# Optimization experiments

Hardware: AMD Instinct MI355X
Metric: run time of the kernel (lower is better)

## Reference

```python
import jax, jax.numpy as jnp
import numpy as np

Nc, Np = 100_000, 200_000
E = 1_000_000
D_IN, C, H = 64, 128, 8
D = C // H  # per-head dim = 16
NEG_SLOPE = 0.2
BN_EPS = 1e-5


def setup_inputs() -> dict:
    key = jax.random.key(0)
    ks = jax.random.split(key, 24)
    rn = lambda i, shape, s=0.05: jax.random.normal(ks[i], shape, jnp.float32) * s
    inp = {
        'x_customer': jax.random.normal(ks[0], (Nc, D_IN), jnp.float32),
        'x_product': jax.random.normal(ks[1], (Np, D_IN), jnp.float32),
        'edge_src_cp': jax.random.randint(ks[2], (E,), 0, Nc),
        'edge_dst_cp': jax.random.randint(ks[3], (E,), 0, Np),
        'edge_src_pp': jax.random.randint(ks[4], (E,), 0, Np),
        'edge_dst_pp': jax.random.randint(ks[5], (E,), 0, Np),
        # HANConv per-node-type projections
        'W_c': rn(6, (D_IN, C)), 'b_c': jnp.zeros((C,), jnp.float32),
        'W_p': rn(7, (D_IN, C)), 'b_p': jnp.zeros((C,), jnp.float32),
        # per-edge-type attention vectors [H, D]
        'a_src_cp': rn(8, (H, D), 0.2), 'a_dst_cp': rn(9, (H, D), 0.2),
        'a_src_pp': rn(10, (H, D), 0.2), 'a_dst_pp': rn(11, (H, D), 0.2),
        # semantic attention (k_lin + q)
        'Wk': rn(12, (C, C)), 'bk': jnp.zeros((C,), jnp.float32),
        'q_sem': rn(13, (C,), 0.2),
        # MLP head + BN params
        'W1': rn(14, (C, 128)), 'b1': jnp.zeros((128,), jnp.float32),
        'g1': jnp.ones((128,), jnp.float32), 'be1': jnp.zeros((128,), jnp.float32),
        'W2': rn(15, (128, 64)), 'b2': jnp.zeros((64,), jnp.float32),
        'g2': jnp.ones((64,), jnp.float32), 'be2': jnp.zeros((64,), jnp.float32),
        'W3': rn(16, (64, 1)), 'b3': jnp.zeros((1,), jnp.float32),
    }
    return inp


def _edge_type_attention(h_src, h_dst, a_src, a_dst, e_src, e_dst, n_dst):
    # h_src: [N_src, H, D]; per-node attention logits [N, H]
    al_src = jnp.sum(h_src * a_src, axis=-1)
    al_dst = jnp.sum(h_dst * a_dst, axis=-1)
    al = al_src[e_src] + al_dst[e_dst]                      # [E, H]
    al = jnp.where(al >= 0, al, NEG_SLOPE * al)             # leaky_relu
    m = jax.ops.segment_max(al, e_dst, num_segments=n_dst)  # [n_dst, H]
    m = jnp.where(jnp.isfinite(m), m, 0.0)                  # empty segments
    ex = jnp.exp(al - m[e_dst])
    s = jax.ops.segment_sum(ex, e_dst, num_segments=n_dst)
    alpha = ex / (s[e_dst] + 1e-16)                         # [E, H]
    msg = h_src[e_src] * alpha[..., None]                   # [E, H, D]
    out = jax.ops.segment_sum(msg, e_dst, num_segments=n_dst)
    return jax.nn.relu(out.reshape(n_dst, H * D))


def _bn(x, g, b):
    mu = jnp.mean(x, axis=0)
    var = jnp.var(x, axis=0)
    return g * (x - mu) * jax.lax.rsqrt(var + BN_EPS) + b


def reference(x_customer, x_product, W_c, b_c, W_p, b_p,
              a_src_cp, a_dst_cp, a_src_pp, a_dst_pp,
              Wk, bk, q_sem,
              W1, b1, g1, be1, W2, b2, g2, be2, W3, b3,
              edge_src_cp, edge_dst_cp, edge_src_pp, edge_dst_pp):
    # node-type projections -> [N, H, D]
    h_c = (x_customer @ W_c + b_c).reshape(Nc, H, D)
    h_p = (x_product @ W_p + b_p).reshape(Np, H, D)
    # per-edge-type multi-head attention into 'product_order'
    out_cp = _edge_type_attention(h_c, h_p, a_src_cp, a_dst_cp, edge_src_cp, edge_dst_cp, Np)
    out_pp = _edge_type_attention(h_p, h_p, a_src_pp, a_dst_pp, edge_src_pp, edge_dst_pp, Np)
    # semantic attention over the 2 metapaths
    outs = jnp.stack([out_cp, out_pp])                      # [2, Np, C]
    k = jnp.mean(jnp.tanh(outs @ Wk + bk), axis=1)          # [2, C]
    attn = jax.nn.softmax(jnp.sum(k * q_sem, axis=-1))      # [2]
    out = jnp.sum(attn[:, None, None] * outs, axis=0)       # [Np, C]
    # MLP head (dropout disabled; BN uses batch statistics)
    h = jax.nn.relu(_bn(out @ W1 + b1, g1, be1))
    h = jax.nn.relu(_bn(h @ W2 + b2, g2, be2))
    return jax.nn.sigmoid(h @ W3 + b3)
```

## Files before the change

### kernel.cpp

```cpp
#include <hip/hip_runtime.h>
#include <hip/hip_bf16.h>

#define NC 100000
#define NP 200000
#define NE 1000000
#define NN2 (2 * NP)
#define NBUK 391
#define ECHUNK 8192
#define NBLK_E 245
#define NTILE 3125
#define SEMB 782

typedef unsigned short u16;
typedef unsigned int u32;
typedef unsigned long long u64;
typedef __attribute__((ext_vector_type(8))) short short8v;
typedef __attribute__((ext_vector_type(4))) float f32x4;

__device__ __forceinline__ float bf2f(u16 v) {
    union { u32 u; float f; } c; c.u = ((u32)v) << 16; return c.f;
}
__device__ __forceinline__ u16 f2bf(float f) {
    union { float f; u32 u; } c; c.f = f;
    u32 u = c.u;
    return (u16)((u + 0x7FFFu + ((u >> 16) & 1u)) >> 16);
}
__device__ __forceinline__ u32 pack2(float lo, float hi) {
    return (u32)f2bf(lo) | ((u32)f2bf(hi) << 16);
}
__device__ __forceinline__ float tanh_fast(float x) {
    return 1.f - 2.f / (__expf(2.f * x) + 1.f);
}
__device__ __forceinline__ short8v mk8(u32 a, u32 b, u32 c, u32 d) {
    union { u32 u[4]; short8v v; } t; t.u[0] = a; t.u[1] = b; t.u[2] = c; t.u[3] = d; return t.v;
}

__global__ __launch_bounds__(256) void proj_both(
    const float* __restrict__ x_c, const float* __restrict__ W_c, const float* __restrict__ b_c,
    const float* __restrict__ x_p, const float* __restrict__ W_p, const float* __restrict__ b_p,
    u16* __restrict__ out_c, u16* __restrict__ out_p,
    const float* __restrict__ a_cp_s,
    const float* __restrict__ a_cp_d, const float* __restrict__ a_pp_s,
    const float* __restrict__ a_pp_d,
    float* __restrict__ al_c, float* __restrict__ al_dcp,
    float* __restrict__ al_spp, float* __restrict__ al_dpp)
{
    const float* x; const float* W; const float* b; u16* h; int N;
    int py = blockIdx.y;
    if (py == 0) { x = x_c; W = W_c; b = b_c; h = out_c; N = NC; }
    else         { x = x_p; W = W_p; b = b_p; h = out_p; N = NP; }
    size_t row0 = (size_t)blockIdx.x * 64;
    if (row0 >= (size_t)N) return;
    __shared__ alignas(16) u16 sBT[128 * 72];
    __shared__ alignas(16) u16 sA[64 * 72];
    __shared__ alignas(16) u16 hTile[64 * 136];
    __shared__ float aV[3][128];
    int t = threadIdx.x;
    if (t < 128) {
        aV[0][t] = py ? a_cp_d[t] : a_cp_s[t];
        aV[1][t] = py ? a_pp_s[t] : 0.f;
        aV[2][t] = py ? a_pp_d[t] : 0.f;
    }
    for (int i = t; i < 128 * 8; i += 256) {
        int n = i & 127, kb = i >> 7;
        u32 p[4];
#pragma unroll
        for (int j = 0; j < 4; ++j)
            p[j] = pack2(W[(kb * 8 + 2 * j) * 128 + n], W[(kb * 8 + 2 * j + 1) * 128 + n]);
        *(uint4*)(&sBT[n * 72 + kb * 8]) = make_uint4(p[0], p[1], p[2], p[3]);
    }
    for (int i = t; i < 64 * 8; i += 256) {
        int r = i >> 3, c8 = (i & 7) * 8;
        u32 p[4];
        if (row0 + r < (size_t)N) {
            const float* src = x + (row0 + r) * 64 + c8;
            float4 v0 = *(const float4*)src;
            float4 v1 = *(const float4*)(src + 4);
            p[0] = pack2(v0.x, v0.y); p[1] = pack2(v0.z, v0.w);
            p[2] = pack2(v1.x, v1.y); p[3] = pack2(v1.z, v1.w);
        } else { p[0] = p[1] = p[2] = p[3] = 0; }
        *(uint4*)(&sA[r * 72 + c8]) = make_uint4(p[0], p[1], p[2], p[3]);
    }
    __syncthreads();
    int wave = t >> 6, lane = t & 63;
    int fr = lane & 15, fq = lane >> 4;
    const u16* pA = sA + (wave * 16 + fr) * 72 + fq * 8;
    const u16* pB = sBT + fr * 72 + fq * 8;
    f32x4 acc[8];
#pragma unroll
    for (int nt = 0; nt < 8; ++nt) { float bb = b[nt * 16 + fr]; acc[nt] = (f32x4){bb, bb, bb, bb}; }
#pragma unroll
    for (int ks = 0; ks < 2; ++ks) {
        short8v a = *(const short8v*)(pA + ks * 32);
#pragma unroll
        for (int nt = 0; nt < 8; ++nt) {
            short8v bv = *(const short8v*)(pB + nt * 16 * 72 + ks * 32);
            acc[nt] = __builtin_amdgcn_mfma_f32_16x16x32_bf16(a, bv, acc[nt], 0, 0, 0);
        }
    }
    size_t rbase = row0 + wave * 16 + fq * 4;
    int lrow0 = wave * 16 + fq * 4;
#pragma unroll
    for (int nt = 0; nt < 8; ++nt) {
        int col = nt * 16 + fr;
#pragma unroll
        for (int rg = 0; rg < 4; ++rg) {
            size_t rr = rbase + rg;
            u16 hv = f2bf(acc[nt][rg]);
            if (rr < (size_t)N) h[rr * 128 + col] = hv;
            hTile[(lrow0 + rg) * 136 + col] = hv;
        }
    }
    __syncthreads();
    int row = t >> 2;
    size_t grow = row0 + row;
    if (grow < (size_t)N) {
#pragma unroll
        for (int hd = t & 3; hd < 8; hd += 4) {
            const u16* hp = &hTile[row * 136 + hd * 16];
            uint4 u0_ = *(const uint4*)hp;
            uint4 u1_ = *(const uint4*)(hp + 8);
            u32 uu[8] = {u0_.x, u0_.y, u0_.z, u0_.w, u1_.x, u1_.y, u1_.z, u1_.w};
            float p0 = 0.f, p1 = 0.f, p2 = 0.f;
#pragma unroll
            for (int j = 0; j < 8; ++j) {
                float lo = bf2f((u16)(uu[j] & 0xFFFFu));
                float hi = bf2f((u16)(uu[j] >> 16));
                int c = hd * 16 + 2 * j;
                p0 += lo * aV[0][c] + hi * aV[0][c + 1];
                p1 += lo * aV[1][c] + hi * aV[1][c + 1];
                p2 += lo * aV[2][c] + hi * aV[2][c + 1];
            }
            if (py == 0) {
                al_c[grow * 8 + hd] = p0;
            } else {
                al_dcp[grow * 8 + hd] = p0;
                al_spp[grow * 8 + hd] = p1;
                al_dpp[grow * 8 + hd] = p2;
            }
        }
    }
}

__global__ __launch_bounds__(256) void bhist(const int* __restrict__ dpp, const int* __restrict__ dcp,
                                             int* __restrict__ bcnt)
{
    __shared__ int h[NBUK];
    int t = threadIdx.x;
    for (int i = t; i < NBUK; i += 256) h[i] = 0;
    __syncthreads();
    int base = blockIdx.x * ECHUNK;
    int lim = min(ECHUNK, 2 * NE - base);
    for (int i = t; i < lim; i += 256) {
        int e = base + i;
        int d2 = (e < NE) ? dpp[e] : NP + dcp[e - NE];
        atomicAdd(&h[d2 >> 10], 1);
    }
    __syncthreads();
    for (int i = t; i < NBUK; i += 256) if (h[i]) atomicAdd(&bcnt[i], h[i]);
}

__global__ __launch_bounds__(512) void bscan(const int* __restrict__ bcnt, int* __restrict__ bbase,
                                             int* __restrict__ bcur, int* __restrict__ row_ptr)
{
    __shared__ int s[512];
    int t = threadIdx.x;
    int v = (t < NBUK) ? bcnt[t] : 0;
    s[t] = v;
    __syncthreads();
    for (int off = 1; off < 512; off <<= 1) {
        int x = (t >= off) ? s[t - off] : 0;
        __syncthreads();
        s[t] += x;
        __syncthreads();
    }
    if (t < NBUK) { bbase[t] = s[t] - v; bcur[t] = s[t] - v; }
    if (t == 0) { bbase[NBUK] = 2 * NE; row_ptr[NN2] = 2 * NE; }
}

__global__ __launch_bounds__(256) void bplace(
    const int* __restrict__ spp, const int* __restrict__ dpp,
    const int* __restrict__ scp, const int* __restrict__ dcp,
    int* __restrict__ bcur, u64* __restrict__ pairs)
{
    __shared__ int h[NBUK];
    __shared__ int rk[NBUK];
    int t = threadIdx.x;
    for (int i = t; i < NBUK; i += 256) h[i] = 0;
    __syncthreads();
    int base = blockIdx.x * ECHUNK;
    int lim = min(ECHUNK, 2 * NE - base);
    for (int i = t; i < lim; i += 256) {
        int e = base + i;
        int d2 = (e < NE) ? dpp[e] : NP + dcp[e - NE];
        atomicAdd(&h[d2 >> 10], 1);
    }
    __syncthreads();
    for (int i = t; i < NBUK; i += 256) {
        int c = h[i];
        h[i] = c ? atomicAdd(&bcur[i], c) : 0;
        rk[i] = 0;
    }
    __syncthreads();
    for (int i = t; i < lim; i += 256) {
        int e = base + i;
        int d2, src;
        if (e < NE) { d2 = dpp[e];      src = spp[e]; }
        else        { d2 = NP + dcp[e - NE]; src = scp[e - NE]; }
        int b = d2 >> 10;
        int r = atomicAdd(&rk[b], 1);
        pairs[h[b] + r] = ((u64)(u32)d2 << 32) | (u32)src;
    }
}

__global__ __launch_bounds__(256) void bsort(
    const u64* __restrict__ pairs, const int* __restrict__ bbase,
    int* __restrict__ row_ptr, int* __restrict__ perm)
{
    __shared__ int cnt[1024];
    __shared__ int sc[256];
    int b = blockIdx.x, t = threadIdx.x;
    int beg = bbase[b], end = bbase[b + 1];
    for (int i = t; i < 1024; i += 256) cnt[i] = 0;
    __syncthreads();
    for (int i = beg + t; i < end; i += 256) {
        int d2 = (int)(pairs[i] >> 32);
        atomicAdd(&cnt[d2 & 1023], 1);
    }
    __syncthreads();
    int b4 = t * 4;
    int c0 = cnt[b4], c1 = cnt[b4 + 1], c2 = cnt[b4 + 2], c3 = cnt[b4 + 3];
    int s = c0 + c1 + c2 + c3;
    sc[t] = s;
    __syncthreads();
    for (int off = 1; off < 256; off <<= 1) {
        int x = (t >= off) ? sc[t - off] : 0;
        __syncthreads();
        sc[t] += x;
        __syncthreads();
    }
    int run = sc[t] - s;
    int o0 = run, o1 = run + c0, o2 = o1 + c1, o3 = o2 + c2;
    cnt[b4] = o0; cnt[b4 + 1] = o1; cnt[b4 + 2] = o2; cnt[b4 + 3] = o3;
    int gidx = b * 1024 + b4;
    if (gidx     < NN2) row_ptr[gidx]     = beg + o0;
    if (gidx + 1 < NN2) row_ptr[gidx + 1] = beg + o1;
    if (gidx + 2 < NN2) row_ptr[gidx + 2] = beg + o2;
    if (gidx + 3 < NN2) row_ptr[gidx + 3] = beg + o3;
    __syncthreads();
    for (int i = beg + t; i < end; i += 256) {
        u64 p = pairs[i];
        int d2 = (int)(p >> 32);
        int r = atomicAdd(&cnt[d2 & 1023], 1);
        perm[beg + r] = (int)(p & 0xFFFFFFFFull);
    }
}

__global__ __launch_bounds__(256) void gather2(
    const int* __restrict__ row_ptr, const int* __restrict__ perm,
    const float* __restrict__ als_pp, const float* __restrict__ ald_pp,
    const float* __restrict__ als_cp, const float* __restrict__ ald_cp,
    const u16* __restrict__ h_p, const u16* __restrict__ h_c,
    u16* __restrict__ r_pp, u16* __restrict__ r_cp)
{
    int d2 = blockIdx.x * 16 + (threadIdx.x >> 4);
    int lane = threadIdx.x & 63;
    int l16 = lane & 15;
    int grp = lane & 48;
    int head = l16 >> 1;
    const float* als; const float* ald; const u16* hs; u16* out; int d;
    if (d2 < NP) { d = d2;      als = als_pp; ald = ald_pp; hs = h_p; out = r_pp; }
    else         { d = d2 - NP; als = als_cp; ald = ald_cp; hs = h_c; out = r_cp; }
    int beg = row_ptr[d2], end = row_ptr[d2 + 1];
    int n = end - beg;
    float ald_h = ald[(size_t)d * 8 + head];
    float dsum = 0.f;
    float acc[8] = {0.f, 0.f, 0.f, 0.f, 0.f, 0.f, 0.f, 0.f};
    for (int base = 0; base < n; base += 16) {
        int cnt = min(16, n - base);
        int my = (base + l16 < n) ? perm[beg + base + l16] : 0;
        int src = __shfl(my, grp, 64);
        float a_next = als[(size_t)src * 8 + head];
        uint4 hv_next = *(const uint4*)(hs + (size_t)src * 128 + l16 * 8);
        for (int j = 0; j < cnt; ++j) {
            float a_cur = a_next;
            uint4 hv = hv_next;
            if (j + 1 < cnt) {
                int s2 = __shfl(my, grp + j + 1, 64);
                a_next = als[(size_t)s2 * 8 + head];
                hv_next = *(const uint4*)(hs + (size_t)s2 * 128 + l16 * 8);
            }
            float a = a_cur + ald_h;
            a = a >= 0.f ? a : 0.2f * a;
            float w = __expf(a);
            dsum += w;
            u32 uu[4] = {hv.x, hv.y, hv.z, hv.w};
#pragma unroll
            for (int q = 0; q < 4; ++q) {
                acc[2 * q]     = fmaf(bf2f((u16)(uu[q] & 0xFFFFu)), w, acc[2 * q]);
                acc[2 * q + 1] = fmaf(bf2f((u16)(uu[q] >> 16)),     w, acc[2 * q + 1]);
            }
        }
    }
    float inv = 1.f / (dsum + 1e-16f);
    uint4 o;
    o.x = pack2(fmaxf(acc[0] * inv, 0.f), fmaxf(acc[1] * inv, 0.f));
    o.y = pack2(fmaxf(acc[2] * inv, 0.f), fmaxf(acc[3] * inv, 0.f));
    o.z = pack2(fmaxf(acc[4] * inv, 0.f), fmaxf(acc[5] * inv, 0.f));
    o.w = pack2(fmaxf(acc[6] * inv, 0.f), fmaxf(acc[7] * inv, 0.f));
    *(uint4*)(out + (size_t)d * 128 + l16 * 8) = o;
}

__global__ __launch_bounds__(256) void sem_mfma(
    const u16* __restrict__ r0, const u16* __restrict__ r1,
    const float* __restrict__ Wk, const float* __restrict__ bk,
    float* __restrict__ part)
{
    __shared__ alignas(16) u16 sBT[128 * 136];
    __shared__ float red[4][128];
    int t = threadIdx.x;
    const u16* src = blockIdx.y ? r1 : r0;
    for (int i = t; i < 128 * 16; i += 256) {
        int n = i & 127, kb = i >> 7;
        u32 p[4];
#pragma unroll
        for (int j = 0; j < 4; ++j)
            p[j] = pack2(Wk[(kb * 8 + 2 * j) * 128 + n], Wk[(kb * 8 + 2 * j + 1) * 128 + n]);
        *(uint4*)(&sBT[n * 136 + kb * 8]) = make_uint4(p[0], p[1], p[2], p[3]);
    }
    __syncthreads();
    int wave = t >> 6, lane = t & 63;
    int fr = lane & 15, fq = lane >> 4;
    const u16* pB = sBT + fr * 136 + fq * 8;
    float bias = bk[fr];
    float sacc[8] = {0.f, 0.f, 0.f, 0.f, 0.f, 0.f, 0.f, 0.f};
    float bkv[8];
#pragma unroll
    for (int nt = 0; nt < 8; ++nt) bkv[nt] = bk[nt * 16 + fr];
    (void)bias;
    for (int ti = 0; ti < 4; ++ti) {
        int tile = blockIdx.x * 4 + ti;
        if (tile >= NTILE) break;
        size_t arow = (size_t)tile * 64 + wave * 16 + fr;
        const u16* ap = src + arow * 128 + fq * 8;
        short8v afr[4];
#pragma unroll
        for (int ks = 0; ks < 4; ++ks) afr[ks] = *(const short8v*)(ap + ks * 32);
        f32x4 acc[8];
#pragma unroll
        for (int nt = 0; nt < 8; ++nt) acc[nt] = (f32x4){bkv[nt], bkv[nt], bkv[nt], bkv[nt]};
#pragma unroll
        for (int ks = 0; ks < 4; ++ks) {
#pragma unroll
            for (int nt = 0; nt < 8; ++nt) {
                short8v bv = *(const short8v*)(pB + nt * 16 * 136 + ks * 32);
                acc[nt] = __builtin_amdgcn_mfma_f32_16x16x32_bf16(afr[ks], bv, acc[nt], 0, 0, 0);
            }
        }
#pragma unroll
        for (int nt = 0; nt < 8; ++nt) {
            f32x4 v = acc[nt];
            sacc[nt] += tanh_fast(v[0]) + tanh_fast(v[1]) + tanh_fast(v[2]) + tanh_fast(v[3]);
        }
    }
#pragma unroll
    for (int nt = 0; nt < 8; ++nt) {
        float s = sacc[nt];
        s += __shfl_xor(s, 16, 64);
        s += __shfl_xor(s, 32, 64);
        if (lane < 16) red[wave][nt * 16 + lane] = s;
    }
    __syncthreads();
    if (t < 128) {
        float s = red[0][t] + red[1][t] + red[2][t] + red[3][t];
        part[((size_t)blockIdx.y * SEMB + blockIdx.x) * 128 + t] = s;
    }
}

__global__ __launch_bounds__(256) void sem_dot(const float* __restrict__ part,
                                               const float* __restrict__ q, float* __restrict__ vsum)
{
    __shared__ float sq_[128];
    __shared__ float red[256];
    int t = threadIdx.x;
    if (t < 128) sq_[t] = q[t];
    __syncthreads();
    int c = t & 127, m = t >> 7;
    int i0 = blockIdx.x * 25;
    int i1 = i0 + 25; if (i1 > SEMB) i1 = SEMB;
    float acc = 0.f;
    for (int i = i0; i < i1; ++i)
        acc += part[((size_t)m * SEMB + i) * 128 + c] * sq_[c];
    red[t] = acc;
    __syncthreads();
    for (int off = 64; off >= 1; off >>= 1) {
        if ((t & 127) < off) red[t] += red[t + off];
        __syncthreads();
    }
    if ((t & 127) == 0) atomicAdd(&vsum[m], red[t]);
}

__global__ __launch_bounds__(256) void mlp1_mfma(
    const u16* __restrict__ rcp, const u16* __restrict__ rpp, const float* __restrict__ vsum,
    const float* __restrict__ W1, const float* __restrict__ b1,
    u16* __restrict__ z1, float* __restrict__ pS, float* __restrict__ pQ)
{
    __shared__ alignas(16) u16 sBT[128 * 136];
    __shared__ float redS[4][128];
    __shared__ float redQ[4][128];
    int t = threadIdx.x;
    float v0 = vsum[0] * (1.f / (float)NP), v1 = vsum[1] * (1.f / (float)NP);
    float mx = fmaxf(v0, v1);
    float e0 = __expf(v0 - mx), e1 = __expf(v1 - mx);
    float is = 1.f / (e0 + e1);
    float a0 = e0 * is, a1 = e1 * is;
    for (int i = t; i < 128 * 16; i += 256) {
        int n = i & 127, kb = i >> 7;
        u32 p[4];
#pragma unroll
        for (int j = 0; j < 4; ++j)
            p[j] = pack2(W1[(kb * 8 + 2 * j) * 128 + n], W1[(kb * 8 + 2 * j + 1) * 128 + n]);
        *(uint4*)(&sBT[n * 136 + kb * 8]) = make_uint4(p[0], p[1], p[2], p[3]);
    }
    __syncthreads();
    int wave = t >> 6, lane = t & 63;
    int fr = lane & 15, fq = lane >> 4;
    const u16* pB = sBT + fr * 136 + fq * 8;
    float b1v[8];
#pragma unroll
    for (int nt = 0; nt < 8; ++nt) b1v[nt] = b1[nt * 16 + fr];
    float saccS[8] = {0.f, 0.f, 0.f, 0.f, 0.f, 0.f, 0.f, 0.f};
    float saccQ[8] = {0.f, 0.f, 0.f, 0.f, 0.f, 0.f, 0.f, 0.f};
    for (int ti = 0; ti < 4; ++ti) {
        int tile = blockIdx.x * 4 + ti;
        if (tile >= NTILE) break;
        size_t row0 = (size_t)tile * 64;
        size_t arow = row0 + wave * 16 + fr;
        const u16* rc = rcp + arow * 128 + fq * 8;
        const u16* rp = rpp + arow * 128 + fq * 8;
        f32x4 acc[8];
#pragma unroll
        for (int nt = 0; nt < 8; ++nt) acc[nt] = (f32x4){b1v[nt], b1v[nt], b1v[nt], b1v[nt]};
#pragma unroll
        for (int ks = 0; ks < 4; ++ks) {
            uint4 uc = *(const uint4*)(rc + ks * 32);
            uint4 up = *(const uint4*)(rp + ks * 32);
            u32 cu[4] = {uc.x, uc.y, uc.z, uc.w};
            u32 pu[4] = {up.x, up.y, up.z, up.w};
            u32 pw[4];
#pragma unroll
            for (int j = 0; j < 4; ++j) {
                float lo = a0 * bf2f((u16)(cu[j] & 0xFFFFu)) + a1 * bf2f((u16)(pu[j] & 0xFFFFu));
                float hi = a0 * bf2f((u16)(cu[j] >> 16))     + a1 * bf2f((u16)(pu[j] >> 16));
                pw[j] = pack2(lo, hi);
            }
            short8v a = mk8(pw[0], pw[1], pw[2], pw[3]);
#pragma unroll
            for (int nt = 0; nt < 8; ++nt) {
                short8v bv = *(const short8v*)(pB + nt * 16 * 136 + ks * 32);
                acc[nt] = __builtin_amdgcn_mfma_f32_16x16x32_bf16(a, bv, acc[nt], 0, 0, 0);
            }
        }
        size_t rbase = row0 + wave * 16 + fq * 4;
#pragma unroll
        for (int nt = 0; nt < 8; ++nt) {
            f32x4 v = acc[nt];
            int col = nt * 16 + fr;
#pragma unroll
            for (int rg = 0; rg < 4; ++rg)
                z1[(rbase + rg) * 128 + col] = f2bf(v[rg]);
            saccS[nt] += v[0] + v[1] + v[2] + v[3];
            saccQ[nt] += v[0] * v[0] + v[1] * v[1] + v[2] * v[2] + v[3] * v[3];
        }
    }
#pragma unroll
    for (int nt = 0; nt < 8; ++nt) {
        float s = saccS[nt], qq = saccQ[nt];
        s += __shfl_xor(s, 16, 64);  s += __shfl_xor(s, 32, 64);
        qq += __shfl_xor(qq, 16, 64); qq += __shfl_xor(qq, 32, 64);
        if (lane < 16) { redS[wave][nt * 16 + lane] = s; redQ[wave][nt * 16 + lane] = qq; }
    }
    __syncthreads();
    if (t < 128) {
        pS[(size_t)blockIdx.x * 128 + t] = redS[0][t] + redS[1][t] + redS[2][t] + redS[3][t];
        pQ[(size_t)blockIdx.x * 128 + t] = redQ[0][t] + redQ[1][t] + redQ[2][t] + redQ[3][t];
    }
}

__global__ __launch_bounds__(256) void stat_reduce(
    const float* __restrict__ pS, const float* __restrict__ pQ,
    float* __restrict__ sum, float* __restrict__ sq, int C)
{
    __shared__ float redS[256], redQ[256];
    int t = threadIdx.x;
    int c = t & (C - 1);
    int sub = t / C;
    int stride = 256 / C;
    int i0 = blockIdx.x * 32, i1 = i0 + 32;
    if (i1 > SEMB) i1 = SEMB;
    float s = 0.f, q = 0.f;
    for (int i = i0 + sub; i < i1; i += stride) {
        s += pS[(size_t)i * C + c];
        q += pQ[(size_t)i * C + c];
    }
    redS[t] = s; redQ[t] = q;
    __syncthreads();
    if (t < C) {
        for (int k = 1; k < stride; ++k) { s += redS[t + k * C]; q += redQ[t + k * C]; }
        atomicAdd(&sum[c], s);
        atomicAdd(&sq[c], q);
    }
}

__global__ __launch_bounds__(256) void mlp2_mfma(
    const u16* __restrict__ z1,
    const float* __restrict__ sum1, const float* __restrict__ sq1,
    const float* __restrict__ g1, const float* __restrict__ be1,
    const float* __restrict__ W2, const float* __restrict__ b2,
    u16* __restrict__ z2, float* __restrict__ pS, float* __restrict__ pQ)
{
    __shared__ alignas(16) u16 sBT[64 * 136];
    __shared__ float sSc[128], sSh[128];
    __shared__ float redS[4][64], redQ[4][64];
    int t = threadIdx.x;
    if (t < 128) {
        float mu = sum1[t] * (1.f / (float)NP);
        float var = sq1[t] * (1.f / (float)NP) - mu * mu;
        float sc = g1[t] * rsqrtf(var + 1e-5f);
        sSc[t] = sc;
        sSh[t] = be1[t] - mu * sc;
    }
    for (int i = t; i < 64 * 16; i += 256) {
        int n = i & 63, kb = i >> 6;
        u32 p[4];
#pragma unroll
        for (int j = 0; j < 4; ++j)
            p[j] = pack2(W2[(kb * 8 + 2 * j) * 64 + n], W2[(kb * 8 + 2 * j + 1) * 64 + n]);
        *(uint4*)(&sBT[n * 136 + kb * 8]) = make_uint4(p[0], p[1], p[2], p[3]);
    }
    __syncthreads();
    int wave = t >> 6, lane = t & 63;
    int fr = lane & 15, fq = lane >> 4;
    const u16* pB = sBT + fr * 136 + fq * 8;
    float b2v[4];
#pragma unroll
    for (int nt = 0; nt < 4; ++nt) b2v[nt] = b2[nt * 16 + fr];
    float sc_[8], sh_[8];
#pragma unroll
    for (int ks = 0; ks < 4; ++ks) {
        int c0 = ks * 32 + fq * 8;
        (void)c0;
    }
    float saccS[4] = {0.f, 0.f, 0.f, 0.f};
    float saccQ[4] = {0.f, 0.f, 0.f, 0.f};
    (void)sc_; (void)sh_;
    for (int ti = 0; ti < 4; ++ti) {
        int tile = blockIdx.x * 4 + ti;
        if (tile >= NTILE) break;
        size_t row0 = (size_t)tile * 64;
        size_t arow = row0 + wave * 16 + fr;
        const u16* zp = z1 + arow * 128 + fq * 8;
        f32x4 acc[4];
#pragma unroll
        for (int nt = 0; nt < 4; ++nt) acc[nt] = (f32x4){b2v[nt], b2v[nt], b2v[nt], b2v[nt]};
#pragma unroll
        for (int ks = 0; ks < 4; ++ks) {
            uint4 uz = *(const uint4*)(zp + ks * 32);
            u32 zu[4] = {uz.x, uz.y, uz.z, uz.w};
            u32 pw[4];
            int c0 = ks * 32 + fq * 8;
#pragma unroll
            for (int j = 0; j < 4; ++j) {
                int c = c0 + 2 * j;
                float lo = fmaxf(bf2f((u16)(zu[j] & 0xFFFFu)) * sSc[c] + sSh[c], 0.f);
                float hi = fmaxf(bf2f((u16)(zu[j] >> 16)) * sSc[c + 1] + sSh[c + 1], 0.f);
                pw[j] = pack2(lo, hi);
            }
            short8v a = mk8(pw[0], pw[1], pw[2], pw[3]);
#pragma unroll
            for (int nt = 0; nt < 4; ++nt) {
                short8v bv = *(const short8v*)(pB + nt * 16 * 136 + ks * 32);
                acc[nt] = __builtin_amdgcn_mfma_f32_16x16x32_bf16(a, bv, acc[nt], 0, 0, 0);
            }
        }
        size_t rbase = row0 + wave * 16 + fq * 4;
#pragma unroll
        for (int nt = 0; nt < 4; ++nt) {
            f32x4 v = acc[nt];
            int col = nt * 16 + fr;
#pragma unroll
            for (int rg = 0; rg < 4; ++rg)
                z2[(rbase + rg) * 64 + col] = f2bf(v[rg]);
            saccS[nt] += v[0] + v[1] + v[2] + v[3];
            saccQ[nt] += v[0] * v[0] + v[1] * v[1] + v[2] * v[2] + v[3] * v[3];
        }
    }
#pragma unroll
    for (int nt = 0; nt < 4; ++nt) {
        float s = saccS[nt], qq = saccQ[nt];
        s += __shfl_xor(s, 16, 64);  s += __shfl_xor(s, 32, 64);
        qq += __shfl_xor(qq, 16, 64); qq += __shfl_xor(qq, 32, 64);
        if (lane < 16) { redS[wave][nt * 16 + lane] = s; redQ[wave][nt * 16 + lane] = qq; }
    }
    __syncthreads();
    if (t < 64) {
        pS[(size_t)blockIdx.x * 64 + t] = redS[0][t] + redS[1][t] + redS[2][t] + redS[3][t];
        pQ[(size_t)blockIdx.x * 64 + t] = redQ[0][t] + redQ[1][t] + redQ[2][t] + redQ[3][t];
    }
}

__global__ __launch_bounds__(64) void final_kernel(
    const u16* __restrict__ z2,
    const float* __restrict__ sum2, const float* __restrict__ sq2,
    const float* __restrict__ g2, const float* __restrict__ be2,
    const float* __restrict__ W3, const float* __restrict__ b3, float* __restrict__ out)
{
    __shared__ float sh[64][65];
    __shared__ float sw[64];
    int t = threadIdx.x;
    float mu = sum2[t] * (1.f / (float)NP);
    float var = sq2[t] * (1.f / (float)NP) - mu * mu;
    float sc = g2[t] * rsqrtf(var + 1e-5f);
    float sh2 = be2[t] - mu * sc;
    size_t row0 = (size_t)blockIdx.x * 64;
    sw[t] = W3[t];
    for (int j = 0; j < 64; ++j) {
        float v = bf2f(z2[(row0 + j) * 64 + t]) * sc + sh2;
        sh[j][t] = v > 0.f ? v : 0.f;
    }
    __syncthreads();
    float acc = b3[0];
#pragma unroll 16
    for (int k = 0; k < 64; ++k) acc = fmaf(sh[t][k], sw[k], acc);
    out[row0 + t] = 1.f / (1.f + __expf(-acc));
}

extern "C" void kernel_launch(void* const* d_in, const int* in_sizes, int n_in,
                              void* d_out, int out_size, void* d_ws, size_t ws_size,
                              hipStream_t stream) {
    const float* x_c      = (const float*)d_in[0];
    const float* x_p      = (const float*)d_in[1];
    const int*   e_src_cp = (const int*)d_in[2];
    const int*   e_dst_cp = (const int*)d_in[3];
    const int*   e_src_pp = (const int*)d_in[4];
    const int*   e_dst_pp = (const int*)d_in[5];
    const float* W_c      = (const float*)d_in[6];
    const float* b_c      = (const float*)d_in[7];
    const float* W_p      = (const float*)d_in[8];
    const float* b_p      = (const float*)d_in[9];
    const float* a_src_cp = (const float*)d_in[10];
    const float* a_dst_cp = (const float*)d_in[11];
    const float* a_src_pp = (const float*)d_in[12];
    const float* a_dst_pp = (const float*)d_in[13];
    const float* Wk       = (const float*)d_in[14];
    const float* bk       = (const float*)d_in[15];
    const float* q_sem    = (const float*)d_in[16];
    const float* W1       = (const float*)d_in[17];
    const float* b1       = (const float*)d_in[18];
    const float* g1       = (const float*)d_in[19];
    const float* be1      = (const float*)d_in[20];
    const float* W2       = (const float*)d_in[21];
    const float* b2       = (const float*)d_in[22];
    const float* g2       = (const float*)d_in[23];
    const float* be2      = (const float*)d_in[24];
    const float* W3       = (const float*)d_in[25];
    const float* b3       = (const float*)d_in[26];

    char* ws = (char*)d_ws;
    u16*   h_p    = (u16*)  (ws +          0);
    u16*   h_c    = (u16*)  (ws +  51200000);
    float* al_c   = (float*)(ws +  76800000);
    float* al_dcp = (float*)(ws +  80000000);
    float* al_spp = (float*)(ws +  86400000);
    float* al_dpp = (float*)(ws +  92800000);
    int*   row_ptr= (int*)  (ws +  99200000);
    int*   perm   = (int*)  (ws + 100800256);
    u64*   pairs  = (u64*)  (ws + 108800256);
    int*   bcnt   = (int*)  (ws + 124800256);
    int*   bbase  = (int*)  (ws + 124801856);
    int*   bcur   = (int*)  (ws + 124803456);
    u16*   r_pp   = (u16*)  (ws + 108800256);
    u16*   r_cp   = (u16*)  (ws + 160000256);
    float* small  = (float*)(ws + 211200256);

    float* semPart= (float*)(ws +  99200000);
    float* statS  = (float*)(ws + 102400000);
    float* statQ  = (float*)(ws + 104000000);

    float* vsum   = small;
    float* sum1   = small + 128;
    float* sq1    = small + 256;
    float* sum2   = small + 384;
    float* sq2    = small + 448;

    u16*   z1 = h_p;
    u16*   z2 = (u16*)(ws + 51200000);

    hipMemsetAsync(small, 0, 8192, stream);
    hipMemsetAsync(bcnt, 0, 1600, stream);

    {
        dim3 g(NP / 64, 2);
        proj_both<<<g, 256, 0, stream>>>(x_c, W_c, b_c, x_p, W_p, b_p, h_c, h_p,
                                         a_src_cp, a_dst_cp, a_src_pp, a_dst_pp,
                                         al_c, al_dcp, al_spp, al_dpp);
    }

    bhist<<<NBLK_E, 256, 0, stream>>>(e_dst_pp, e_dst_cp, bcnt);
    bscan<<<1, 512, 0, stream>>>(bcnt, bbase, bcur, row_ptr);
    bplace<<<NBLK_E, 256, 0, stream>>>(e_src_pp, e_dst_pp, e_src_cp, e_dst_cp, bcur, pairs);
    bsort<<<NBUK, 256, 0, stream>>>(pairs, bbase, row_ptr, perm);

    gather2<<<NN2 / 16, 256, 0, stream>>>(row_ptr, perm,
                                          al_spp, al_dpp, al_c, al_dcp,
                                          h_p, h_c, r_pp, r_cp);

    {
        dim3 gs(SEMB, 2);
        sem_mfma<<<gs, 256, 0, stream>>>(r_cp, r_pp, Wk, bk, semPart);
    }
    sem_dot<<<32, 256, 0, stream>>>(semPart, q_sem, vsum);

    mlp1_mfma<<<SEMB, 256, 0, stream>>>(r_cp, r_pp, vsum, W1, b1, z1, statS, statQ);
    stat_reduce<<<25, 256, 0, stream>>>(statS, statQ, sum1, sq1, 128);
    mlp2_mfma<<<SEMB, 256, 0, stream>>>(z1, sum1, sq1, g1, be1, W2, b2, z2, statS, statQ);
    stat_reduce<<<25, 256, 0, stream>>>(statS, statQ, sum2, sq2, 64);
    final_kernel<<<NP / 64, 64, 0, stream>>>(z2, sum2, sq2, g2, be2, W3, b3, (float*)d_out);
}
```

Before: 394.6 us.

## Fuse histogram into projection, fold sem_dot into sem_mfma, coarsen tile loops

```diff
diff --git a/kernel.cpp b/kernel.cpp
--- a/kernel.cpp
+++ b/kernel.cpp
@@ -9,7 +9,9 @@
 #define ECHUNK 8192
 #define NBLK_E 245
 #define NTILE 3125
-#define SEMB 782
+#define NB8 391
+#define NBLK_PC 391
+#define NBLK_PP 782
 
 typedef unsigned short u16;
 typedef unsigned int u32;
@@ -43,19 +45,37 @@
     const float* __restrict__ a_cp_d, const float* __restrict__ a_pp_s,
     const float* __restrict__ a_pp_d,
     float* __restrict__ al_c, float* __restrict__ al_dcp,
-    float* __restrict__ al_spp, float* __restrict__ al_dpp)
-{
+    float* __restrict__ al_spp, float* __restrict__ al_dpp,
+    const int* __restrict__ dpp, const int* __restrict__ dcp, int* __restrict__ bcnt)
+{
+    __shared__ alignas(16) u16 sBT[128 * 72];
+    __shared__ alignas(16) u16 hTile[64 * 136];
+    __shared__ float aV[3][128];
+    __shared__ int hh[NBUK];
+    int t = threadIdx.x;
+    int py = blockIdx.y;
+    int bx = blockIdx.x;
+
+    if (py == 0 && bx >= NBLK_PC) {
+        int bb = bx - NBLK_PC;
+        if (bb >= NBLK_E) return;
+        for (int i = t; i < NBUK; i += 256) hh[i] = 0;
+        __syncthreads();
+        int base = bb * ECHUNK;
+        int lim = min(ECHUNK, 2 * NE - base);
+        for (int i = t; i < lim; i += 256) {
+            int e = base + i;
+            int d2 = (e < NE) ? dpp[e] : NP + dcp[e - NE];
+            atomicAdd(&hh[d2 >> 10], 1);
+        }
+        __syncthreads();
+        for (int i = t; i < NBUK; i += 256) if (hh[i]) atomicAdd(&bcnt[i], hh[i]);
+        return;
+    }
+
     const float* x; const float* W; const float* b; u16* h; int N;
-    int py = blockIdx.y;
     if (py == 0) { x = x_c; W = W_c; b = b_c; h = out_c; N = NC; }
     else         { x = x_p; W = W_p; b = b_p; h = out_p; N = NP; }
-    size_t row0 = (size_t)blockIdx.x * 64;
-    if (row0 >= (size_t)N) return;
-    __shared__ alignas(16) u16 sBT[128 * 72];
-    __shared__ alignas(16) u16 sA[64 * 72];
-    __shared__ alignas(16) u16 hTile[64 * 136];
-    __shared__ float aV[3][128];
-    int t = threadIdx.x;
     if (t < 128) {
         aV[0][t] = py ? a_cp_d[t] : a_cp_s[t];
         aV[1][t] = py ? a_pp_s[t] : 0.f;
@@ -69,95 +89,84 @@
             p[j] = pack2(W[(kb * 8 + 2 * j) * 128 + n], W[(kb * 8 + 2 * j + 1) * 128 + n]);
         *(uint4*)(&sBT[n * 72 + kb * 8]) = make_uint4(p[0], p[1], p[2], p[3]);
     }
-    for (int i = t; i < 64 * 8; i += 256) {
-        int r = i >> 3, c8 = (i & 7) * 8;
-        u32 p[4];
-        if (row0 + r < (size_t)N) {
-            const float* src = x + (row0 + r) * 64 + c8;
-            float4 v0 = *(const float4*)src;
-            float4 v1 = *(const float4*)(src + 4);
-            p[0] = pack2(v0.x, v0.y); p[1] = pack2(v0.z, v0.w);
-            p[2] = pack2(v1.x, v1.y); p[3] = pack2(v1.z, v1.w);
-        } else { p[0] = p[1] = p[2] = p[3] = 0; }
-        *(uint4*)(&sA[r * 72 + c8]) = make_uint4(p[0], p[1], p[2], p[3]);
-    }
     __syncthreads();
     int wave = t >> 6, lane = t & 63;
     int fr = lane & 15, fq = lane >> 4;
-    const u16* pA = sA + (wave * 16 + fr) * 72 + fq * 8;
     const u16* pB = sBT + fr * 72 + fq * 8;
-    f32x4 acc[8];
-#pragma unroll
-    for (int nt = 0; nt < 8; ++nt) { float bb = b[nt * 16 + fr]; acc[nt] = (f32x4){bb, bb, bb, bb}; }
-#pragma unroll
-    for (int ks = 0; ks < 2; ++ks) {
-        short8v a = *(const short8v*)(pA + ks * 32);
+    float bv8[8];
+#pragma unroll
+    for (int nt = 0; nt < 8; ++nt) bv8[nt] = b[nt * 16 + fr];
+
+    for (int ti = 0; ti < 4; ++ti) {
+        size_t row0 = ((size_t)bx * 4 + ti) * 64;
+        if (row0 >= (size_t)N) break;
+        size_t arow = row0 + wave * 16 + fr;
+        short8v afr[2];
+#pragma unroll
+        for (int ks = 0; ks < 2; ++ks) {
+            if (arow < (size_t)N) {
+                const float* xp = x + arow * 64 + ks * 32 + fq * 8;
+                float4 v0 = *(const float4*)xp;
+                float4 v1 = *(const float4*)(xp + 4);
+                afr[ks] = mk8(pack2(v0.x, v0.y), pack2(v0.z, v0.w),
+                              pack2(v1.x, v1.y), pack2(v1.z, v1.w));
+            } else afr[ks] = mk8(0, 0, 0, 0);
+        }
+        f32x4 acc[8];
+#pragma unroll
+        for (int nt = 0; nt < 8; ++nt) acc[nt] = (f32x4){bv8[nt], bv8[nt], bv8[nt], bv8[nt]};
+#pragma unroll
+        for (int ks = 0; ks < 2; ++ks) {
+#pragma unroll
+            for (int nt = 0; nt < 8; ++nt) {
+                short8v bv = *(const short8v*)(pB + nt * 16 * 72 + ks * 32);
+                acc[nt] = __builtin_amdgcn_mfma_f32_16x16x32_bf16(afr[ks], bv, acc[nt], 0, 0, 0);
+            }
+        }
+        size_t rbase = row0 + wave * 16 + fq * 4;
+        int lrow0 = wave * 16 + fq * 4;
 #pragma unroll
         for (int nt = 0; nt < 8; ++nt) {
-            short8v bv = *(const short8v*)(pB + nt * 16 * 72 + ks * 32);
-            acc[nt] = __builtin_amdgcn_mfma_f32_16x16x32_bf16(a, bv, acc[nt], 0, 0, 0);
-        }
-    }
-    size_t rbase = row0 + wave * 16 + fq * 4;
-    int lrow0 = wave * 16 + fq * 4;
-#pragma unroll
-    for (int nt = 0; nt < 8; ++nt) {
-        int col = nt * 16 + fr;
-#pragma unroll
-        for (int rg = 0; rg < 4; ++rg) {
-            size_t rr = rbase + rg;
-            u16 hv = f2bf(acc[nt][rg]);
-            if (rr < (size_t)N) h[rr * 128 + col] = hv;
-            hTile[(lrow0 + rg) * 136 + col] = hv;
-        }
-    }
-    __syncthreads();
-    int row = t >> 2;
-    size_t grow = row0 + row;
-    if (grow < (size_t)N) {
-#pragma unroll
-        for (int hd = t & 3; hd < 8; hd += 4) {
-            const u16* hp = &hTile[row * 136 + hd * 16];
-            uint4 u0_ = *(const uint4*)hp;
-            uint4 u1_ = *(const uint4*)(hp + 8);
-            u32 uu[8] = {u0_.x, u0_.y, u0_.z, u0_.w, u1_.x, u1_.y, u1_.z, u1_.w};
-            float p0 = 0.f, p1 = 0.f, p2 = 0.f;
-#pragma unroll
-            for (int j = 0; j < 8; ++j) {
-                float lo = bf2f((u16)(uu[j] & 0xFFFFu));
-                float hi = bf2f((u16)(uu[j] >> 16));
-                int c = hd * 16 + 2 * j;
-                p0 += lo * aV[0][c] + hi * aV[0][c + 1];
-                p1 += lo * aV[1][c] + hi * aV[1][c + 1];
-                p2 += lo * aV[2][c] + hi * aV[2][c + 1];
-            }
-            if (py == 0) {
-                al_c[grow * 8 + hd] = p0;
-            } else {
-                al_dcp[grow * 8 + hd] = p0;
-                al_spp[grow * 8 + hd] = p1;
-                al_dpp[grow * 8 + hd] = p2;
-            }
-        }
-    }
-}
-
-__global__ __launch_bounds__(256) void bhist(const int* __restrict__ dpp, const int* __restrict__ dcp,
-                                             int* __restrict__ bcnt)
-{
-    __shared__ int h[NBUK];
-    int t = threadIdx.x;
-    for (int i = t; i < NBUK; i += 256) h[i] = 0;
-    __syncthreads();
-    int base = blockIdx.x * ECHUNK;
-    int lim = min(ECHUNK, 2 * NE - base);
-    for (int i = t; i < lim; i += 256) {
-        int e = base + i;
-        int d2 = (e < NE) ? dpp[e] : NP + dcp[e - NE];
-        atomicAdd(&h[d2 >> 10], 1);
-    }
-    __syncthreads();
-    for (int i = t; i < NBUK; i += 256) if (h[i]) atomicAdd(&bcnt[i], h[i]);
+            int col = nt * 16 + fr;
+#pragma unroll
+            for (int rg = 0; rg < 4; ++rg) {
+                size_t rr = rbase + rg;
+                u16 hv = f2bf(acc[nt][rg]);
+                if (rr < (size_t)N) h[rr * 128 + col] = hv;
+                hTile[(lrow0 + rg) * 136 + col] = hv;
+            }
+        }
+        __syncthreads();
+        int row = t >> 2;
+        size_t grow = row0 + row;
+        if (grow < (size_t)N) {
+#pragma unroll
+            for (int hd = t & 3; hd < 8; hd += 4) {
+                const u16* hp = &hTile[row * 136 + hd * 16];
+                uint4 u0_ = *(const uint4*)hp;
+                uint4 u1_ = *(const uint4*)(hp + 8);
+                u32 uu[8] = {u0_.x, u0_.y, u0_.z, u0_.w, u1_.x, u1_.y, u1_.z, u1_.w};
+                float p0 = 0.f, p1 = 0.f, p2 = 0.f;
+#pragma unroll
+                for (int j = 0; j < 8; ++j) {
+                    float lo = bf2f((u16)(uu[j] & 0xFFFFu));
+                    float hi = bf2f((u16)(uu[j] >> 16));
+                    int c = hd * 16 + 2 * j;
+                    p0 += lo * aV[0][c] + hi * aV[0][c + 1];
+                    p1 += lo * aV[1][c] + hi * aV[1][c + 1];
+                    p2 += lo * aV[2][c] + hi * aV[2][c + 1];
+                }
+                if (py == 0) {
+                    al_c[grow * 8 + hd] = p0;
+                } else {
+                    al_dcp[grow * 8 + hd] = p0;
+                    al_spp[grow * 8 + hd] = p1;
+                    al_dpp[grow * 8 + hd] = p2;
+                }
+            }
+        }
+        __syncthreads();
+    }
 }
 
 __global__ __launch_bounds__(512) void bscan(const int* __restrict__ bcnt, int* __restrict__ bbase,
@@ -314,12 +323,15 @@
 __global__ __launch_bounds__(256) void sem_mfma(
     const u16* __restrict__ r0, const u16* __restrict__ r1,
     const float* __restrict__ Wk, const float* __restrict__ bk,
-    float* __restrict__ part)
+    const float* __restrict__ q, float* __restrict__ vsum)
 {
     __shared__ alignas(16) u16 sBT[128 * 136];
     __shared__ float red[4][128];
+    __shared__ float sq_[128];
+    __shared__ float dotb[128];
     int t = threadIdx.x;
     const u16* src = blockIdx.y ? r1 : r0;
+    if (t < 128) sq_[t] = q[t];
     for (int i = t; i < 128 * 16; i += 256) {
         int n = i & 127, kb = i >> 7;
         u32 p[4];
@@ -332,14 +344,12 @@
     int wave = t >> 6, lane = t & 63;
     int fr = lane & 15, fq = lane >> 4;
     const u16* pB = sBT + fr * 136 + fq * 8;
-    float bias = bk[fr];
+    float bkv[8];
+#pragma unroll
+    for (int nt = 0; nt < 8; ++nt) bkv[nt] = bk[nt * 16 + fr];
     float sacc[8] = {0.f, 0.f, 0.f, 0.f, 0.f, 0.f, 0.f, 0.f};
-    float bkv[8];
-#pragma unroll
-    for (int nt = 0; nt < 8; ++nt) bkv[nt] = bk[nt * 16 + fr];
-    (void)bias;
-    for (int ti = 0; ti < 4; ++ti) {
-        int tile = blockIdx.x * 4 + ti;
+    for (int ti = 0; ti < 8; ++ti) {
+        int tile = blockIdx.x * 8 + ti;
         if (tile >= NTILE) break;
         size_t arow = (size_t)tile * 64 + wave * 16 + fr;
         const u16* ap = src + arow * 128 + fq * 8;
@@ -371,33 +381,14 @@
         if (lane < 16) red[wave][nt * 16 + lane] = s;
     }
     __syncthreads();
-    if (t < 128) {
-        float s = red[0][t] + red[1][t] + red[2][t] + red[3][t];
-        part[((size_t)blockIdx.y * SEMB + blockIdx.x) * 128 + t] = s;
-    }
-}
-
-__global__ __launch_bounds__(256) void sem_dot(const float* __restrict__ part,
-                                               const float* __restrict__ q, float* __restrict__ vsum)
-{
-    __shared__ float sq_[128];
-    __shared__ float red[256];
-    int t = threadIdx.x;
-    if (t < 128) sq_[t] = q[t];
-    __syncthreads();
-    int c = t & 127, m = t >> 7;
-    int i0 = blockIdx.x * 25;
-    int i1 = i0 + 25; if (i1 > SEMB) i1 = SEMB;
-    float acc = 0.f;
-    for (int i = i0; i < i1; ++i)
-        acc += part[((size_t)m * SEMB + i) * 128 + c] * sq_[c];
-    red[t] = acc;
-    __syncthreads();
-    for (int off = 64; off >= 1; off >>= 1) {
-        if ((t & 127) < off) red[t] += red[t + off];
-        __syncthreads();
-    }
-    if ((t & 127) == 0) atomicAdd(&vsum[m], red[t]);
+    if (t < 128) dotb[t] = (red[0][t] + red[1][t] + red[2][t] + red[3][t]) * sq_[t];
+    __syncthreads();
+    if (t < 64) {
+        float v = dotb[t] + dotb[t + 64];
+#pragma unroll
+        for (int off = 32; off >= 1; off >>= 1) v += __shfl_xor(v, off, 64);
+        if (t == 0) atomicAdd(&vsum[blockIdx.y], v);
+    }
 }
 
 __global__ __launch_bounds__(256) void mlp1_mfma(
@@ -431,8 +422,8 @@
     for (int nt = 0; nt < 8; ++nt) b1v[nt] = b1[nt * 16 + fr];
     float saccS[8] = {0.f, 0.f, 0.f, 0.f, 0.f, 0.f, 0.f, 0.f};
     float saccQ[8] = {0.f, 0.f, 0.f, 0.f, 0.f, 0.f, 0.f, 0.f};
-    for (int ti = 0; ti < 4; ++ti) {
-        int tile = blockIdx.x * 4 + ti;
+    for (int ti = 0; ti < 8; ++ti) {
+        int tile = blockIdx.x * 8 + ti;
         if (tile >= NTILE) break;
         size_t row0 = (size_t)tile * 64;
         size_t arow = row0 + wave * 16 + fr;
@@ -496,8 +487,8 @@
     int c = t & (C - 1);
     int sub = t / C;
     int stride = 256 / C;
-    int i0 = blockIdx.x * 32, i1 = i0 + 32;
-    if (i1 > SEMB) i1 = SEMB;
+    int i0 = blockIdx.x * 25, i1 = i0 + 25;
+    if (i1 > NB8) i1 = NB8;
     float s = 0.f, q = 0.f;
     for (int i = i0 + sub; i < i1; i += stride) {
         s += pS[(size_t)i * C + c];
@@ -545,17 +536,10 @@
     float b2v[4];
 #pragma unroll
     for (int nt = 0; nt < 4; ++nt) b2v[nt] = b2[nt * 16 + fr];
-    float sc_[8], sh_[8];
-#pragma unroll
-    for (int ks = 0; ks < 4; ++ks) {
-        int c0 = ks * 32 + fq * 8;
-        (void)c0;
-    }
     float saccS[4] = {0.f, 0.f, 0.f, 0.f};
     float saccQ[4] = {0.f, 0.f, 0.f, 0.f};
-    (void)sc_; (void)sh_;
-    for (int ti = 0; ti < 4; ++ti) {
-        int tile = blockIdx.x * 4 + ti;
+    for (int ti = 0; ti < 8; ++ti) {
+        int tile = blockIdx.x * 8 + ti;
         if (tile >= NTILE) break;
         size_t row0 = (size_t)tile * 64;
         size_t arow = row0 + wave * 16 + fr;
@@ -683,7 +667,6 @@
     u16*   r_cp   = (u16*)  (ws + 160000256);
     float* small  = (float*)(ws + 211200256);
 
-    float* semPart= (float*)(ws +  99200000);
     float* statS  = (float*)(ws + 102400000);
     float* statQ  = (float*)(ws + 104000000);
 
@@ -700,13 +683,13 @@
     hipMemsetAsync(bcnt, 0, 1600, stream);
 
     {
-        dim3 g(NP / 64, 2);
+        dim3 g(NBLK_PP, 2);
         proj_both<<<g, 256, 0, stream>>>(x_c, W_c, b_c, x_p, W_p, b_p, h_c, h_p,
                                          a_src_cp, a_dst_cp, a_src_pp, a_dst_pp,
-                                         al_c, al_dcp, al_spp, al_dpp);
-    }
-
-    bhist<<<NBLK_E, 256, 0, stream>>>(e_dst_pp, e_dst_cp, bcnt);
+                                         al_c, al_dcp, al_spp, al_dpp,
+                                         e_dst_pp, e_dst_cp, bcnt);
+    }
+
     bscan<<<1, 512, 0, stream>>>(bcnt, bbase, bcur, row_ptr);
     bplace<<<NBLK_E, 256, 0, stream>>>(e_src_pp, e_dst_pp, e_src_cp, e_dst_cp, bcur, pairs);
     bsort<<<NBUK, 256, 0, stream>>>(pairs, bbase, row_ptr, perm);
@@ -716,14 +699,13 @@
                                           h_p, h_c, r_pp, r_cp);
 
     {
-        dim3 gs(SEMB, 2);
-        sem_mfma<<<gs, 256, 0, stream>>>(r_cp, r_pp, Wk, bk, semPart);
-    }
-    sem_dot<<<32, 256, 0, stream>>>(semPart, q_sem, vsum);
-
-    mlp1_mfma<<<SEMB, 256, 0, stream>>>(r_cp, r_pp, vsum, W1, b1, z1, statS, statQ);
-    stat_reduce<<<25, 256, 0, stream>>>(statS, statQ, sum1, sq1, 128);
-    mlp2_mfma<<<SEMB, 256, 0, stream>>>(z1, sum1, sq1, g1, be1, W2, b2, z2, statS, statQ);
-    stat_reduce<<<25, 256, 0, stream>>>(statS, statQ, sum2, sq2, 64);
+        dim3 gs(NB8, 2);
+        sem_mfma<<<gs, 256, 0, stream>>>(r_cp, r_pp, Wk, bk, q_sem, vsum);
+    }
+
+    mlp1_mfma<<<NB8, 256, 0, stream>>>(r_cp, r_pp, vsum, W1, b1, z1, statS, statQ);
+    stat_reduce<<<16, 256, 0, stream>>>(statS, statQ, sum1, sq1, 128);
+    mlp2_mfma<<<NB8, 256, 0, stream>>>(z1, sum1, sq1, g1, be1, W2, b2, z2, statS, statQ);
+    stat_reduce<<<16, 256, 0, stream>>>(statS, statQ, sum2, sq2, 64);
     final_kernel<<<NP / 64, 64, 0, stream>>>(z2, sum2, sq2, g2, be2, W3, b3, (float*)d_out);
 }
```

Result: faster. 366.5 us (-7.1%).
